# Performance work log

Hardware: AMD Instinct MI355X
Metric: run time of the kernel (lower is better)

Reference implementation:

```python
import jax, jax.numpy as jnp
import numpy as np

N = 2048
HID = 1024
Z = 256
DIM = 128 + 64 * 3 + 32 * 5  # 480
FAN = 128 * 128 + 64 * 64 + 32 * 32  # total fan-in over all CG paths


def _ln(x, g, b, eps=1e-6):
    mu = jnp.mean(x, axis=-1, keepdims=True)
    var = jnp.mean((x - mu) ** 2, axis=-1, keepdims=True)
    return (x - mu) * jax.lax.rsqrt(var + eps) * g + b


def _fctp(t, w0, w1, w2):
    # FullyConnectedTensorProduct(irreps, irreps, 'HIDx0e'):
    # only l1==l2 -> 0e paths survive; CG is delta_{m1,m2}/sqrt(2l+1).
    x0 = t[:, :128]                       # 128x0e
    x1 = t[:, 128:320].reshape(-1, 64, 3)  # 64x1o
    x2 = t[:, 320:480].reshape(-1, 32, 5)  # 32x2e
    e0 = jnp.einsum('bu,bv,uvh->bh', x0, x0, w0)
    e1 = jnp.einsum('bum,bvm,uvh->bh', x1, x1, w1) / np.sqrt(3.0)
    e2 = jnp.einsum('bum,bvm,uvh->bh', x2, x2, w2) / np.sqrt(5.0)
    return (e0 + e1 + e2) / np.sqrt(float(FAN))  # component normalization


def _head(t, w0, w1, w2, W1, b1, g1, be1, W2, b2, g2, be2):
    h = _fctp(t, w0, w1, w2)
    h = jax.nn.silu(_ln(h @ W1 + b1, g1, be1))
    h = jax.nn.silu(_ln(h @ W2 + b2, g2, be2))
    return h  # [N, Z]


def setup_inputs() -> dict:
    key = jax.random.key(0)
    ks = jax.random.split(key, 6)
    return {
        'tensor_in': jax.random.normal(ks[0], (N, DIM), jnp.float32),
        'w0': jax.random.normal(ks[1], (128, 128, HID), jnp.float32),
        'w1': jax.random.normal(ks[2], (64, 64, HID), jnp.float32),
        'w2': jax.random.normal(ks[3], (32, 32, HID), jnp.float32),
        'W1': jax.random.normal(ks[4], (HID, HID), jnp.float32) / np.sqrt(HID),
        'b1': jnp.zeros((HID,), jnp.float32),
        'g1': jnp.ones((HID,), jnp.float32),
        'be1': jnp.zeros((HID,), jnp.float32),
        'W2': jax.random.normal(ks[5], (HID, Z), jnp.float32) / np.sqrt(HID),
        'b2': jnp.zeros((Z,), jnp.float32),
        'g2': jnp.ones((Z,), jnp.float32),
        'be2': jnp.zeros((Z,), jnp.float32),
    }


def reference(tensor_in, w0, w1, w2, W1, b1, g1, be1, W2, b2, g2, be2):
    f = lambda t: _head(t, w0, w1, w2, W1, b1, g1, be1, W2, b2, g2, be2)
    x, pullback = jax.vjp(f, tensor_in)
    # torch: grad(x, tensor_in, grad_outputs=ones_like(x), create_graph=True)
    y = pullback(jnp.ones_like(x))[0]
    return x, y
```

## Files before the change

kernel.cpp:

```cpp
#include <hip/hip_runtime.h>
#include <math.h>

typedef unsigned short u16;
typedef __bf16 bf16x8 __attribute__((ext_vector_type(8)));
typedef float f32x4 __attribute__((ext_vector_type(4)));

#define NPACK  11264
#define NVALID 10864
#define BASE1  8256
#define BASE2  10336

__device__ __forceinline__ u16 f2bf(float f) {
    unsigned u = __builtin_bit_cast(unsigned, f);
    u += 0x7FFFu + ((u >> 16) & 1u);
    return (u16)(u >> 16);
}
__device__ __forceinline__ float bf2f(u16 h) {
    return __builtin_bit_cast(float, ((unsigned)h) << 16);
}

#define GLOAD_LDS16(g, l)                                                     \
    __builtin_amdgcn_global_load_lds(                                         \
        (const __attribute__((address_space(1))) void*)(g),                   \
        (__attribute__((address_space(3))) void*)(l), 16, 0, 0)

__device__ __forceinline__ int pk0(int a, int b) {
    int u = min(a, b), v = max(a, b);
    return u * 128 - (u * (u - 1)) / 2 + (v - u);
}
__device__ __forceinline__ int pk1(int a, int b) {
    int u = min(a, b), v = max(a, b);
    return BASE1 + u * 64 - (u * (u - 1)) / 2 + (v - u);
}
__device__ __forceinline__ int pk2(int a, int b) {
    int u = min(a, b), v = max(a, b);
    return BASE2 + u * 32 - (u * (u - 1)) / 2 + (v - u);
}

__global__ __launch_bounds__(256) void k_uvall(u16* __restrict__ tab) {
    int j = blockIdx.x * 256 + threadIdx.x;
    if (j < 16384) {
        int u = j >> 7, v = j & 127;
        if (v >= u) tab[pk0(u, v)] = (u16)((u << 7) | v);
    } else if (j < 20480) {
        int k = j - 16384, u = k >> 6, v = k & 63;
        if (v >= u) tab[pk1(u, v)] = (u16)((1 << 14) | (u << 7) | v);
    } else if (j < 21504) {
        int k = j - 20480, u = k >> 5, v = k & 31;
        if (v >= u) tab[pk2(u, v)] = (u16)((2 << 14) | (u << 7) | v);
    } else {
        int k = j - 21504;
        if (NVALID + k < NPACK) tab[NVALID + k] = 0xFFFFu;
    }
}

__global__ __launch_bounds__(256) void k_packw(const float* __restrict__ w0,
                                               const float* __restrict__ w1,
                                               const float* __restrict__ w2,
                                               const u16* __restrict__ tab,
                                               u16* __restrict__ Wsym,
                                               u16* __restrict__ Wt) {
    __shared__ u16 tile[32][258];
    __shared__ u16 te[32];
    int i0 = blockIdx.x * 32, h0 = blockIdx.y * 256, tid = threadIdx.x;
    if (tid < 32) te[tid] = tab[i0 + tid];
    __syncthreads();
    const float s1 = 0.57735026918962576f, s2 = 0.44721359549995794f;
    for (int il = 0; il < 32; il++) {
        unsigned e = te[il];
        float val = 0.f;
        if ((e >> 14) != 3) {
            int seg = e >> 14, u = (e >> 7) & 127, v = e & 127;
            const float* wb; int S; float sc;
            if (seg == 0)      { wb = w0; S = 128; sc = 1.f; }
            else if (seg == 1) { wb = w1; S = 64;  sc = s1; }
            else               { wb = w2; S = 32;  sc = s2; }
            val = sc * (wb[(size_t)(u * S + v) * 1024 + h0 + tid] +
                        wb[(size_t)(v * S + u) * 1024 + h0 + tid]);
        }
        u16 bv = f2bf(val);
        Wsym[(size_t)(i0 + il) * 1024 + h0 + tid] = bv;
        tile[il][tid] = bv;
    }
    __syncthreads();
    union { u16 a[32]; uint4 q[4]; } pk;
#pragma unroll
    for (int il = 0; il < 32; il++) pk.a[il] = tile[il][tid];
    uint4* dst = (uint4*)(Wt + (size_t)(h0 + tid) * NPACK + i0);
#pragma unroll
    for (int q = 0; q < 4; q++) dst[q] = pk.q[q];
}

__global__ __launch_bounds__(256) void k_convert(const float* __restrict__ in,
                                                 u16* __restrict__ out, int n4) {
    int i = blockIdx.x * 256 + threadIdx.x;
    if (i >= n4) return;
    float4 v = ((const float4*)in)[i];
    union { u16 a[4]; unsigned long long q; } o;
    o.a[0] = f2bf(v.x); o.a[1] = f2bf(v.y); o.a[2] = f2bf(v.z); o.a[3] = f2bf(v.w);
    ((unsigned long long*)out)[i] = o.q;
}

__global__ __launch_bounds__(256) void k_transpose(const float* __restrict__ in, int R, int C,
                                                   u16* __restrict__ out, int ldOut) {
    __shared__ float tile[32][33];
    int tr0 = blockIdx.y * 32;
    int tc0 = blockIdx.x * 32;
    int lr = threadIdx.x >> 5;
    int lc = threadIdx.x & 31;
#pragma unroll
    for (int i = 0; i < 4; i++) {
        int rr = lr + i * 8;
        tile[rr][lc] = in[(size_t)(tr0 + rr) * C + tc0 + lc];
    }
    __syncthreads();
#pragma unroll
    for (int i = 0; i < 4; i++) {
        int rr = lr + i * 8;
        out[(size_t)(tc0 + rr) * ldOut + tr0 + lc] = f2bf(tile[lc][rr]);
    }
}

__global__ __launch_bounds__(256) void k_features_pack(const float* __restrict__ t,
                                                       const u16* __restrict__ tab,
                                                       u16* __restrict__ P) {
    __shared__ u16 tab_s[NPACK];
    __shared__ float tr[480];
    int b = blockIdx.x, tid = threadIdx.x;
    for (int j = tid; j < NPACK / 8; j += 256)
        ((uint4*)tab_s)[j] = ((const uint4*)tab)[j];
    for (int j = tid; j < 480; j += 256) tr[j] = t[(size_t)b * 480 + j];
    __syncthreads();
    u16* row = P + (size_t)b * NPACK;
    for (int i = tid; i < NPACK; i += 256) {
        unsigned e = tab_s[i];
        float p = 0.f;
        if ((e >> 14) != 3) {
            int seg = e >> 14, u = (e >> 7) & 127, v = e & 127;
            if (seg == 0) p = tr[u] * tr[v];
            else if (seg == 1) {
                const float* x1 = tr + 128;
                p = x1[u*3]*x1[v*3] + x1[u*3+1]*x1[v*3+1] + x1[u*3+2]*x1[v*3+2];
            } else {
                const float* x2 = tr + 320;
#pragma unroll
                for (int m = 0; m < 5; m++) p += x2[u*5+m] * x2[v*5+m];
            }
            if (u == v) p *= 0.5f;
        }
        row[i] = f2bf(p);
    }
}

__global__ __launch_bounds__(256) void k_gemm2(const u16* __restrict__ A, int ldA,
                                               const u16* __restrict__ B, int ldB,
                                               int kLen, float scale,
                                               const float* __restrict__ bias,
                                               float* __restrict__ Cf,
                                               u16* __restrict__ Cb, int ldC,
                                               float* __restrict__ Cpart, int Mtot,
                                               int swz) {
    __shared__ u16 As[2][128 * 32];
    __shared__ u16 Bs[2][128 * 32];
    const int tid = threadIdx.x;
    const int wave = tid >> 6, lane = tid & 63;
    const int wm = wave >> 1, wn = wave & 1;
    int nT, mT, z;
    if (swz == 1) {
        int L = blockIdx.x;
        z = L & 7; int r = L >> 3;
        nT = r >> 4; mT = r & 15;
    } else if (swz == 2) {
        int L = blockIdx.x;
        int c = L & 7, r = L >> 3;
        nT = (r % 11) * 8 + c; mT = r / 11; z = 0;
    } else {
        nT = blockIdx.x; mT = blockIdx.y; z = blockIdx.z;
    }
    const int m0 = mT * 128, n0 = nT * 128;
    const size_t kOff = (size_t)z * kLen;

    const int chl = (((lane & 3) ^ ((lane >> 3) & 3))) * 8;
    const u16* aG = A + (size_t)(m0 + wave * 32 + (lane >> 2)) * ldA + kOff + chl;
    const u16* bG = B + (size_t)(n0 + wave * 32 + (lane >> 2)) * ldB + kOff + chl;
    const size_t aS = (size_t)16 * ldA;
    const size_t bS = (size_t)16 * ldB;
    u16* aL0 = &As[0][(wave * 32) * 32];
    u16* aL1 = &As[0][(wave * 32 + 16) * 32];
    u16* aH0 = &As[1][(wave * 32) * 32];
    u16* aH1 = &As[1][(wave * 32 + 16) * 32];
    u16* bL0 = &Bs[0][(wave * 32) * 32];
    u16* bL1 = &Bs[0][(wave * 32 + 16) * 32];
    u16* bH0 = &Bs[1][(wave * 32) * 32];
    u16* bH1 = &Bs[1][(wave * 32 + 16) * 32];

    f32x4 acc[4][4];
#pragma unroll
    for (int i = 0; i < 4; i++)
#pragma unroll
        for (int j = 0; j < 4; j++) acc[i][j] = (f32x4){0.f, 0.f, 0.f, 0.f};

    const int ml = lane & 15, kq8 = lane >> 4;
    const int kqs = (kq8 ^ ((ml >> 1) & 3)) * 8;
    const u16* aRd0 = &As[0][(wm * 64 + ml) * 32 + kqs];
    const u16* bRd0 = &Bs[0][(wn * 64 + ml) * 32 + kqs];
    const u16* aRd1 = &As[1][(wm * 64 + ml) * 32 + kqs];
    const u16* bRd1 = &Bs[1][(wn * 64 + ml) * 32 + kqs];

    for (int k = 0; k < kLen; k += 64) {
        GLOAD_LDS16(aG, aL0);
        GLOAD_LDS16(aG + aS, aL1);
        GLOAD_LDS16(aG + 32, aH0);
        GLOAD_LDS16(aG + aS + 32, aH1);
        GLOAD_LDS16(bG, bL0);
        GLOAD_LDS16(bG + bS, bL1);
        GLOAD_LDS16(bG + 32, bH0);
        GLOAD_LDS16(bG + bS + 32, bH1);
        aG += 64; bG += 64;
        __syncthreads();
        {
            bf16x8 af[4], bfv[4];
#pragma unroll
            for (int i = 0; i < 4; i++) af[i]  = *(const bf16x8*)(aRd0 + i * 16 * 32);
#pragma unroll
            for (int j = 0; j < 4; j++) bfv[j] = *(const bf16x8*)(bRd0 + j * 16 * 32);
#pragma unroll
            for (int i = 0; i < 4; i++)
#pragma unroll
                for (int j = 0; j < 4; j++)
                    acc[i][j] = __builtin_amdgcn_mfma_f32_16x16x32_bf16(af[i], bfv[j], acc[i][j], 0, 0, 0);
        }
        {
            bf16x8 af[4], bfv[4];
#pragma unroll
            for (int i = 0; i < 4; i++) af[i]  = *(const bf16x8*)(aRd1 + i * 16 * 32);
#pragma unroll
            for (int j = 0; j < 4; j++) bfv[j] = *(const bf16x8*)(bRd1 + j * 16 * 32);
#pragma unroll
            for (int i = 0; i < 4; i++)
#pragma unroll
                for (int j = 0; j < 4; j++)
                    acc[i][j] = __builtin_amdgcn_mfma_f32_16x16x32_bf16(af[i], bfv[j], acc[i][j], 0, 0, 0);
        }
        __syncthreads();
    }

    const int q = lane >> 4, nl = lane & 15;
    if (Cpart) {
        float* outP = Cpart + (size_t)z * Mtot * ldC;
#pragma unroll
        for (int i = 0; i < 4; i++)
#pragma unroll
            for (int j = 0; j < 4; j++)
#pragma unroll
                for (int reg = 0; reg < 4; reg++) {
                    int row = m0 + wm * 64 + i * 16 + q * 4 + reg;
                    int col = n0 + wn * 64 + j * 16 + nl;
                    outP[(size_t)row * ldC + col] = acc[i][j][reg];
                }
    } else {
#pragma unroll
        for (int i = 0; i < 4; i++)
#pragma unroll
            for (int j = 0; j < 4; j++)
#pragma unroll
                for (int reg = 0; reg < 4; reg++) {
                    int row = m0 + wm * 64 + i * 16 + q * 4 + reg;
                    int col = n0 + wn * 64 + j * 16 + nl;
                    float v = acc[i][j][reg] * scale + (bias ? bias[col] : 0.0f);
                    if (Cf) Cf[(size_t)row * ldC + col] = v;
                    else    Cb[(size_t)row * ldC + col] = f2bf(v);
                }
    }
}

#define VMCNT0 asm volatile("s_waitcnt vmcnt(0)" ::: "memory")
#define BARX() __builtin_amdgcn_s_barrier()

#define STG_A(p, kh, rh, kb) GLOAD_LDS16(aB + (size_t)(rh) * aH + (kb) + (kh) * 32, \
                                         &As[p][kh][((rh) * 128 + wave * 16) * 32])
#define STG_B(p, kh, rh, kb) GLOAD_LDS16(bB + (size_t)(rh) * bH + (kb) + (kh) * 32, \
                                         &Bs[p][kh][((rh) * 128 + wave * 16) * 32])
#define MMQ(fb, gb, bv) do { _Pragma("unroll") \
    for (int ff = 0; ff < 4; ff++) { _Pragma("unroll") \
        for (int gg = 0; gg < 2; gg++) { \
            acc[(fb)+ff][(gb)+gg] = __builtin_amdgcn_mfma_f32_16x16x32_bf16(a[2*ff],   bv[2*gg],   acc[(fb)+ff][(gb)+gg], 0, 0, 0); \
            acc[(fb)+ff][(gb)+gg] = __builtin_amdgcn_mfma_f32_16x16x32_bf16(a[2*ff+1], bv[2*gg+1], acc[(fb)+ff][(gb)+gg], 0, 0, 0); } } } while (0)

__global__ __launch_bounds__(512, 2) void k_gemm256(const u16* __restrict__ A, int ldA,
                                                    const u16* __restrict__ B, int ldB,
                                                    int kLen, float scale,
                                                    const float* __restrict__ bias,
                                                    u16* __restrict__ Cb, int ldC,
                                                    float* __restrict__ Cpart, int Mtot,
                                                    int swz) {
    __shared__ __align__(16) u16 As[2][2][256 * 32];
    __shared__ __align__(16) u16 Bs[2][2][256 * 32];
    const int tid = threadIdx.x;
    const int lane = tid & 63, wave = tid >> 6;
    const int wm = wave >> 2, wn = wave & 3;
    int mT, nT, z;
    if (swz == 1) {
        z = blockIdx.x & 7; int r = blockIdx.x >> 3; nT = r & 3; mT = r >> 2;
    } else {
        int x = blockIdx.x & 7, j = blockIdx.x >> 3;
        int nti = j >> 3; mT = j & 7;
        if (nti < 5)      nT = nti * 8 + x;
        else if (x < 4)   nT = 40 + x;
        else            { nT = 40 + (x - 4); mT = (j & 7) + 4; }
        z = 0;
    }
    const int m0 = mT * 256, n0 = nT * 256;
    const size_t kOff = (size_t)z * kLen;
    const int nTi = kLen >> 6;

    const int chl = ((tid & 3) ^ ((tid >> 3) & 3)) * 8;
    const u16* aB = A + (size_t)(m0 + (tid >> 2)) * ldA + kOff + chl;
    const u16* bB = B + (size_t)(n0 + (tid >> 2)) * ldB + kOff + chl;
    const size_t aH = (size_t)128 * ldA;
    const size_t bH = (size_t)128 * ldB;

    const int ml = lane & 15, kq8 = lane >> 4;
    const int kqs = (kq8 ^ ((ml >> 1) & 3)) * 8;
    const int aro = (wm * 128 + ml) * 32 + kqs;
    const int bro = (wn * 64 + ml) * 32 + kqs;

    f32x4 acc[8][4];
#pragma unroll
    for (int f = 0; f < 8; f++)
#pragma unroll
        for (int g = 0; g < 4; g++) acc[f][g] = (f32x4){0.f, 0.f, 0.f, 0.f};
    bf16x8 a[8], b[4], b2[4];

    STG_A(0, 0, 0, 0); STG_A(0, 0, 1, 0); STG_A(0, 1, 0, 0); STG_A(0, 1, 1, 0);
    STG_B(0, 0, 0, 0); STG_B(0, 0, 1, 0); STG_B(0, 1, 0, 0); STG_B(0, 1, 1, 0);
    VMCNT0;
    BARX();

    for (int t = 0; t < nTi; t++) {
        const int p = t & 1, p1 = p ^ 1;
        const int kb1 = (t + 1) << 6;
        const bool s1 = (t + 1) < nTi;
#pragma unroll
        for (int f = 0; f < 4; f++) {
            a[2*f]   = *(const bf16x8*)&As[p][0][aro + f * 512];
            a[2*f+1] = *(const bf16x8*)&As[p][1][aro + f * 512];
        }
#pragma unroll
        for (int g = 0; g < 2; g++) {
            b[2*g]   = *(const bf16x8*)&Bs[p][0][bro + g * 512];
            b[2*g+1] = *(const bf16x8*)&Bs[p][1][bro + g * 512];
        }
        if (s1) { STG_A(p1, 0, 0, kb1); STG_A(p1, 0, 1, kb1); }
        BARX();
        __builtin_amdgcn_s_setprio(1);
        MMQ(0, 0, b);
        __builtin_amdgcn_s_setprio(0);
        BARX();
#pragma unroll
        for (int g = 0; g < 2; g++) {
            b2[2*g]   = *(const bf16x8*)&Bs[p][0][bro + (g + 2) * 512];
            b2[2*g+1] = *(const bf16x8*)&Bs[p][1][bro + (g + 2) * 512];
        }
        if (s1) { STG_A(p1, 1, 0, kb1); STG_A(p1, 1, 1, kb1); }
        BARX();
        __builtin_amdgcn_s_setprio(1);
        MMQ(0, 2, b2);
        __builtin_amdgcn_s_setprio(0);
        BARX();
#pragma unroll
        for (int f = 0; f < 4; f++) {
            a[2*f]   = *(const bf16x8*)&As[p][0][aro + (f + 4) * 512];
            a[2*f+1] = *(const bf16x8*)&As[p][1][aro + (f + 4) * 512];
        }
        if (s1) { STG_B(p1, 0, 0, kb1); STG_B(p1, 0, 1, kb1); }
        BARX();
        __builtin_amdgcn_s_setprio(1);
        MMQ(4, 0, b);
        __builtin_amdgcn_s_setprio(0);
        BARX();
        if (s1) { STG_B(p1, 1, 0, kb1); STG_B(p1, 1, 1, kb1); }
        __builtin_amdgcn_s_setprio(1);
        MMQ(4, 2, b2);
        __builtin_amdgcn_s_setprio(0);
        if (s1) VMCNT0;
        BARX();
    }

    const int q = lane >> 4, nl = lane & 15;
    if (Cpart) {
        float* outP = Cpart + (size_t)z * Mtot * ldC;
#pragma unroll
        for (int f = 0; f < 8; f++)
#pragma unroll
            for (int g = 0; g < 4; g++)
#pragma unroll
                for (int reg = 0; reg < 4; reg++) {
                    int row = m0 + wm * 128 + f * 16 + q * 4 + reg;
                    int col = n0 + wn * 64 + g * 16 + nl;
                    outP[(size_t)row * ldC + col] = acc[f][g][reg];
                }
    } else {
#pragma unroll
        for (int f = 0; f < 8; f++)
#pragma unroll
            for (int g = 0; g < 4; g++)
#pragma unroll
                for (int reg = 0; reg < 4; reg++) {
                    int row = m0 + wm * 128 + f * 16 + q * 4 + reg;
                    int col = n0 + wn * 64 + g * 16 + nl;
                    float v = acc[f][g][reg] * scale + (bias ? bias[col] : 0.0f);
                    Cb[(size_t)row * ldC + col] = f2bf(v);
                }
    }
}

__global__ __launch_bounds__(256) void k_reduce(const float* __restrict__ part, size_t stride,
                                                int SK, int total, int N, float scale,
                                                const float* __restrict__ bias,
                                                float* __restrict__ outF, u16* __restrict__ outB) {
    int i = blockIdx.x * 256 + threadIdx.x;
    if (i >= total) return;
    float s = 0.f;
    for (int z = 0; z < SK; z++) s += part[(size_t)z * stride + i];
    float v = s * scale + (bias ? bias[i % N] : 0.0f);
    if (outF) outF[i] = v;
    else      outB[i] = f2bf(v);
}

__device__ __forceinline__ float blockReduce(float v, float* red) {
#pragma unroll
    for (int off = 32; off > 0; off >>= 1) v += __shfl_down(v, off);
    __syncthreads();
    if ((threadIdx.x & 63) == 0) red[threadIdx.x >> 6] = v;
    __syncthreads();
    return red[0] + red[1] + red[2] + red[3];
}

__global__ __launch_bounds__(256) void k_ln_fwd(const float* __restrict__ X, int D,
    const float* __restrict__ g, const float* __restrict__ be,
    float* __restrict__ mu_out, float* __restrict__ r_out,
    u16* __restrict__ a_bf, float* __restrict__ a_f32) {
    __shared__ float red[4];
    int b = blockIdx.x, tid = threadIdx.x;
    const float* x = X + (size_t)b * D;
    int nd = D >> 8;
    float s = 0.f, s2 = 0.f;
    for (int r = 0; r < nd; r++) { float v = x[tid + (r << 8)]; s += v; s2 += v * v; }
    s = blockReduce(s, red);
    s2 = blockReduce(s2, red);
    float mu = s / D;
    float var = s2 / D - mu * mu;
    float rst = rsqrtf(var + 1e-6f);
    if (tid == 0) { mu_out[b] = mu; r_out[b] = rst; }
    for (int r = 0; r < nd; r++) {
        int i = tid + (r << 8);
        float xh = (x[i] - mu) * rst;
        float ln = xh * g[i] + be[i];
        float a = ln / (1.0f + expf(-ln));
        if (a_bf)  a_bf[(size_t)b * D + i] = f2bf(a);
        if (a_f32) a_f32[(size_t)b * D + i] = a;
    }
}

__global__ __launch_bounds__(256) void k_ln_bwd(const float* __restrict__ dup,
    const float* __restrict__ X, const float* __restrict__ mu_in, const float* __restrict__ r_in,
    const float* __restrict__ g, const float* __restrict__ be,
    u16* __restrict__ out_bf, int D) {
    __shared__ float red[4];
    int b = blockIdx.x, tid = threadIdx.x;
    const float* x = X + (size_t)b * D;
    float mu = mu_in[b], rst = r_in[b];
    int nd = D >> 8;
    float w_[4], xh_[4];
    float sw = 0.f, swx = 0.f;
    for (int r = 0; r < nd; r++) {
        int i = tid + (r << 8);
        float xh = (x[i] - mu) * rst;
        float ln = xh * g[i] + be[i];
        float sg = 1.0f / (1.0f + expf(-ln));
        float dsilu = sg * (1.0f + ln * (1.0f - sg));
        float d = dup ? dup[(size_t)b * D + i] : 1.0f;
        float w = g[i] * dsilu * d;
        w_[r] = w; xh_[r] = xh;
        sw += w; swx += w * xh;
    }
    sw = blockReduce(sw, red);
    swx = blockReduce(swx, red);
    float invD = 1.0f / D;
    for (int r = 0; r < nd; r++) {
        int i = tid + (r << 8);
        float dx = rst * (w_[r] - sw * invD - xh_[r] * swx * invD);
        out_bf[(size_t)b * D + i] = f2bf(dx);
    }
}

__global__ __launch_bounds__(256) void k_contract_p(const u16* __restrict__ Gp,
                                                    const float* __restrict__ t,
                                                    float* __restrict__ y) {
    __shared__ u16 gp_s[NPACK];
    __shared__ float xs[480];
    int b = blockIdx.x, tid = threadIdx.x;
    const uint4* gsrc = (const uint4*)(Gp + (size_t)b * NPACK);
    for (int j = tid; j < NPACK / 8; j += 256) ((uint4*)gp_s)[j] = gsrc[j];
    for (int j = tid; j < 480; j += 256) xs[j] = t[(size_t)b * 480 + j];
    __syncthreads();
    int wave = tid >> 6, lane = tid & 63;
    float* yr = y + (size_t)b * 480;
    for (int r = 0; r < 32; r++) {
        int u = wave * 32 + r;
        int v0 = lane, v1 = lane + 64;
        float s = bf2f(gp_s[pk0(u, v0)]) * xs[v0] + bf2f(gp_s[pk0(u, v1)]) * xs[v1];
#pragma unroll
        for (int off = 32; off > 0; off >>= 1) s += __shfl_down(s, off);
        if (lane == 0) yr[u] = s;
    }
    for (int r = 0; r < 16; r++) {
        int u = wave * 16 + r;
        float gv = bf2f(gp_s[pk1(u, lane)]);
        float a0 = gv * xs[128 + lane * 3 + 0];
        float a1 = gv * xs[128 + lane * 3 + 1];
        float a2 = gv * xs[128 + lane * 3 + 2];
#pragma unroll
        for (int off = 32; off > 0; off >>= 1) {
            a0 += __shfl_down(a0, off);
            a1 += __shfl_down(a1, off);
            a2 += __shfl_down(a2, off);
        }
        if (lane == 0) {
            yr[128 + u * 3 + 0] = a0;
            yr[128 + u * 3 + 1] = a1;
            yr[128 + u * 3 + 2] = a2;
        }
    }
    for (int r = 0; r < 8; r++) {
        int u = wave * 8 + r;
        bool act = lane < 32;
        float gv = act ? bf2f(gp_s[pk2(u, act ? lane : 0)]) : 0.f;
        float a[5];
#pragma unroll
        for (int m = 0; m < 5; m++)
            a[m] = act ? gv * xs[320 + lane * 5 + m] : 0.f;
#pragma unroll
        for (int off = 32; off > 0; off >>= 1)
#pragma unroll
            for (int m = 0; m < 5; m++) a[m] += __shfl_down(a[m], off);
        if (lane == 0)
#pragma unroll
            for (int m = 0; m < 5; m++) yr[320 + u * 5 + m] = a[m];
    }
}

extern "C" void kernel_launch(void* const* d_in, const int* in_sizes, int n_in,
                              void* d_out, int out_size, void* d_ws, size_t ws_size,
                              hipStream_t stream) {
    const float* t   = (const float*)d_in[0];
    const float* w0  = (const float*)d_in[1];
    const float* w1  = (const float*)d_in[2];
    const float* w2  = (const float*)d_in[3];
    const float* W1  = (const float*)d_in[4];
    const float* b1  = (const float*)d_in[5];
    const float* g1  = (const float*)d_in[6];
    const float* be1 = (const float*)d_in[7];
    const float* W2  = (const float*)d_in[8];
    const float* b2  = (const float*)d_in[9];
    const float* g2  = (const float*)d_in[10];
    const float* be2 = (const float*)d_in[11];

    float* xout = (float*)d_out;
    float* yout = xout + (size_t)2048 * 256;

    char* ws = (char*)d_ws;
    size_t off = 0;
    auto alloc = [&](size_t bytes) -> void* {
        void* p = ws + off;
        off += (bytes + 255) & ~(size_t)255;
        return p;
    };
    u16*   PG    = (u16*)alloc((size_t)2048 * NPACK * 2);
    u16*   Wsym  = (u16*)alloc((size_t)NPACK * 1024 * 2);
    u16*   Wt    = (u16*)alloc((size_t)1024 * NPACK * 2);
    u16*   uvtab = (u16*)alloc((size_t)NPACK * 2);
    u16*   W1b   = (u16*)alloc((size_t)1024 * 1024 * 2);
    u16*   W1tb  = (u16*)alloc((size_t)1024 * 1024 * 2);
    u16*   W2b   = (u16*)alloc((size_t)1024 * 256 * 2);
    u16*   W2tb  = (u16*)alloc((size_t)256 * 1024 * 2);
    u16*   h_bf  = (u16*)alloc((size_t)2048 * 1024 * 2);
    float* h1pre = (float*)alloc((size_t)2048 * 1024 * 4);
    float* mu1   = (float*)alloc(2048 * 4);
    float* r1    = (float*)alloc(2048 * 4);
    u16*   a1_bf = (u16*)alloc((size_t)2048 * 1024 * 2);
    float* h2pre = (float*)alloc((size_t)2048 * 256 * 4);
    float* mu2   = (float*)alloc(2048 * 4);
    float* r2    = (float*)alloc(2048 * 4);
    u16*   dh2b  = (u16*)alloc((size_t)2048 * 256 * 2);
    float* d_a1  = (float*)alloc((size_t)2048 * 1024 * 4);
    u16*   dh1b  = (u16*)alloc((size_t)2048 * 1024 * 2);
    u16*   de_bf = (u16*)alloc((size_t)2048 * 1024 * 2);
    float* Cpart = (float*)(ws + off);
    size_t cpartBytes = (ws_size > off) ? (ws_size - off) : 0;
    (void)in_sizes; (void)n_in; (void)out_size;

    const float sF = 1.0f / sqrtf(21504.0f);

    auto gemm = [&](const u16* A, int ldA, const u16* B, int ldB, int M, int N, int K,
                    int SKwant, float scale, const float* bias,
                    float* Cf, u16* Cb, int ldC) {
        int SK = SKwant;
        size_t slice = (size_t)M * ldC * 4;
        if (SK > 1 && cpartBytes < 2 * slice) SK = 1;
        if (SK > 1 && (size_t)SK * slice > cpartBytes) SK = (int)(cpartBytes / slice);
        while (SK > 1 && !((K % SK) == 0 && ((K / SK) % 64) == 0)) SK--;
        dim3 grid(N / 128, M / 128, SK);
        if (SK > 1) {
            k_gemm2<<<grid, 256, 0, stream>>>(A, ldA, B, ldB, K / SK, 0.f, nullptr,
                                              nullptr, nullptr, ldC, Cpart, M, 0);
            int total = M * ldC;
            k_reduce<<<(total + 255) / 256, 256, 0, stream>>>(Cpart, (size_t)M * ldC, SK,
                                                              total, N, scale, bias, Cf, Cb);
        } else {
            k_gemm2<<<grid, 256, 0, stream>>>(A, ldA, B, ldB, K, scale, bias,
                                              Cf, Cb, ldC, nullptr, M, 0);
        }
    };

    k_uvall<<<(21504 + NPACK - NVALID + 255) / 256, 256, 0, stream>>>(uvtab);
    k_packw<<<dim3(NPACK / 32, 4), 256, 0, stream>>>(w0, w1, w2, uvtab, Wsym, Wt);

    k_transpose<<<dim3(32, 32), 256, 0, stream>>>(W1, 1024, 1024, W1tb, 1024);
    k_transpose<<<dim3(8, 32), 256, 0, stream>>>(W2, 1024, 256, W2tb, 1024);
    k_convert<<<1024 * 1024 / 1024, 256, 0, stream>>>(W1, W1b, 1024 * 1024 / 4);
    k_convert<<<1024 * 256 / 1024, 256, 0, stream>>>(W2, W2b, 1024 * 256 / 4);

    k_features_pack<<<2048, 256, 0, stream>>>(t, uvtab, PG);

    k_gemm256<<<dim3(256), 512, 0, stream>>>(PG, NPACK, Wt, NPACK, NPACK / 8, 0.f, nullptr,
                                             nullptr, 1024, Cpart, 2048, 1);
    {
        int total = 2048 * 1024;
        k_reduce<<<(total + 255) / 256, 256, 0, stream>>>(Cpart, (size_t)2048 * 1024, 8,
                                                          total, 1024, sF, nullptr,
                                                          nullptr, h_bf);
    }

    gemm(h_bf, 1024, W1tb, 1024, 2048, 1024, 1024, 4, 1.0f, b1, h1pre, nullptr, 1024);
    k_ln_fwd<<<2048, 256, 0, stream>>>(h1pre, 1024, g1, be1, mu1, r1, a1_bf, nullptr);
    gemm(a1_bf, 1024, W2tb, 1024, 2048, 256, 1024, 8, 1.0f, b2, h2pre, nullptr, 256);
    k_ln_fwd<<<2048, 256, 0, stream>>>(h2pre, 256, g2, be2, mu2, r2, nullptr, xout);

    k_ln_bwd<<<2048, 256, 0, stream>>>(nullptr, h2pre, mu2, r2, g2, be2, dh2b, 256);
    gemm(dh2b, 256, W2b, 256, 2048, 1024, 256, 4, 1.0f, nullptr, d_a1, nullptr, 1024);
    k_ln_bwd<<<2048, 256, 0, stream>>>(d_a1, h1pre, mu1, r1, g1, be1, dh1b, 1024);
    gemm(dh1b, 1024, W1b, 1024, 2048, 1024, 1024, 4, sF, nullptr, nullptr, de_bf, 1024);

    u16* Gp = PG;
    k_gemm256<<<dim3(352), 512, 0, stream>>>(de_bf, 1024, Wsym, 1024, 1024, 1.0f, nullptr,
                                             Gp, NPACK, nullptr, 2048, 2);

    k_contract_p<<<2048, 256, 0, stream>>>(Gp, t, yout);
}
```

Baseline: 515.7 us.

## Merge weight prep kernels into one launch and store split-K partials as bf16

Five small preprocessing launches (index table, W1/W2 transposes and conversions) become a single kernel that picks its role from the block index, cutting launch overhead. Separately, the split-K GEMM partial sums are now written and read as bf16 instead of fp32, halving partial-buffer traffic. This also changes the workspace sizing so more split slices may fit. The cost is extra rounding of each partial before reduction, which lowers accuracy.

```diff
diff --git a/kernel.cpp b/kernel.cpp
--- a/kernel.cpp
+++ b/kernel.cpp
@@ -37,20 +37,65 @@
     return BASE2 + u * 32 - (u * (u - 1)) / 2 + (v - u);
 }
 
-__global__ __launch_bounds__(256) void k_uvall(u16* __restrict__ tab) {
-    int j = blockIdx.x * 256 + threadIdx.x;
-    if (j < 16384) {
-        int u = j >> 7, v = j & 127;
-        if (v >= u) tab[pk0(u, v)] = (u16)((u << 7) | v);
-    } else if (j < 20480) {
-        int k = j - 16384, u = k >> 6, v = k & 63;
-        if (v >= u) tab[pk1(u, v)] = (u16)((1 << 14) | (u << 7) | v);
-    } else if (j < 21504) {
-        int k = j - 20480, u = k >> 5, v = k & 31;
-        if (v >= u) tab[pk2(u, v)] = (u16)((2 << 14) | (u << 7) | v);
+__device__ __forceinline__ void prep_transpose(const float* __restrict__ in, int C,
+                                               u16* __restrict__ out, int ldOut,
+                                               int bx, int by, int tid) {
+    __shared__ float tile[32][33];
+    int tr0 = by * 32, tc0 = bx * 32;
+    int lr = tid >> 5, lc = tid & 31;
+#pragma unroll
+    for (int i = 0; i < 4; i++) {
+        int rr = lr + i * 8;
+        tile[rr][lc] = in[(size_t)(tr0 + rr) * C + tc0 + lc];
+    }
+    __syncthreads();
+#pragma unroll
+    for (int i = 0; i < 4; i++) {
+        int rr = lr + i * 8;
+        out[(size_t)(tc0 + rr) * ldOut + tr0 + lc] = f2bf(tile[lc][rr]);
+    }
+}
+__device__ __forceinline__ void prep_convert(const float* __restrict__ in,
+                                             u16* __restrict__ out, int i, int n4) {
+    if (i >= n4) return;
+    float4 v = ((const float4*)in)[i];
+    union { u16 a[4]; unsigned long long q; } o;
+    o.a[0] = f2bf(v.x); o.a[1] = f2bf(v.y); o.a[2] = f2bf(v.z); o.a[3] = f2bf(v.w);
+    ((unsigned long long*)out)[i] = o.q;
+}
+
+__global__ __launch_bounds__(256) void k_prep(u16* __restrict__ tab,
+                                              const float* __restrict__ W1,
+                                              const float* __restrict__ W2,
+                                              u16* __restrict__ W1b,
+                                              u16* __restrict__ W1tb,
+                                              u16* __restrict__ W2b,
+                                              u16* __restrict__ W2tb) {
+    int bid = blockIdx.x, tid = threadIdx.x;
+    if (bid < 86) {
+        int j = bid * 256 + tid;
+        if (j < 16384) {
+            int u = j >> 7, v = j & 127;
+            if (v >= u) tab[pk0(u, v)] = (u16)((u << 7) | v);
+        } else if (j < 20480) {
+            int k = j - 16384, u = k >> 6, v = k & 63;
+            if (v >= u) tab[pk1(u, v)] = (u16)((1 << 14) | (u << 7) | v);
+        } else if (j < 21504) {
+            int k = j - 20480, u = k >> 5, v = k & 31;
+            if (v >= u) tab[pk2(u, v)] = (u16)((2 << 14) | (u << 7) | v);
+        } else if (j < 21504 + (NPACK - NVALID)) {
+            tab[NVALID + (j - 21504)] = 0xFFFFu;
+        }
+    } else if (bid < 1110) {
+        int k = bid - 86;
+        prep_transpose(W1, 1024, W1tb, 1024, k & 31, k >> 5, tid);
+    } else if (bid < 1366) {
+        int k = bid - 1110;
+        prep_transpose(W2, 256, W2tb, 1024, k & 7, k >> 3, tid);
+    } else if (bid < 2390) {
+        prep_convert(W1, W1b, (bid - 1366) * 256 + tid, 1024 * 1024 / 4);
     } else {
-        int k = j - 21504;
-        if (NVALID + k < NPACK) tab[NVALID + k] = 0xFFFFu;
+        prep_convert(W2, W2b, (bid - 2390) * 256 + tid, 1024 * 256 / 4);
     }
 }
 
@@ -91,36 +136,6 @@
     for (int q = 0; q < 4; q++) dst[q] = pk.q[q];
 }
 
-__global__ __launch_bounds__(256) void k_convert(const float* __restrict__ in,
-                                                 u16* __restrict__ out, int n4) {
-    int i = blockIdx.x * 256 + threadIdx.x;
-    if (i >= n4) return;
-    float4 v = ((const float4*)in)[i];
-    union { u16 a[4]; unsigned long long q; } o;
-    o.a[0] = f2bf(v.x); o.a[1] = f2bf(v.y); o.a[2] = f2bf(v.z); o.a[3] = f2bf(v.w);
-    ((unsigned long long*)out)[i] = o.q;
-}
-
-__global__ __launch_bounds__(256) void k_transpose(const float* __restrict__ in, int R, int C,
-                                                   u16* __restrict__ out, int ldOut) {
-    __shared__ float tile[32][33];
-    int tr0 = blockIdx.y * 32;
-    int tc0 = blockIdx.x * 32;
-    int lr = threadIdx.x >> 5;
-    int lc = threadIdx.x & 31;
-#pragma unroll
-    for (int i = 0; i < 4; i++) {
-        int rr = lr + i * 8;
-        tile[rr][lc] = in[(size_t)(tr0 + rr) * C + tc0 + lc];
-    }
-    __syncthreads();
-#pragma unroll
-    for (int i = 0; i < 4; i++) {
-        int rr = lr + i * 8;
-        out[(size_t)(tc0 + rr) * ldOut + tr0 + lc] = f2bf(tile[lc][rr]);
-    }
-}
-
 __global__ __launch_bounds__(256) void k_features_pack(const float* __restrict__ t,
                                                        const u16* __restrict__ tab,
                                                        u16* __restrict__ P) {
@@ -158,7 +173,7 @@
                                                const float* __restrict__ bias,
                                                float* __restrict__ Cf,
                                                u16* __restrict__ Cb, int ldC,
-                                               float* __restrict__ Cpart, int Mtot,
+                                               u16* __restrict__ Cpart, int Mtot,
                                                int swz) {
     __shared__ u16 As[2][128 * 32];
     __shared__ u16 Bs[2][128 * 32];
@@ -247,7 +262,7 @@
 
     const int q = lane >> 4, nl = lane & 15;
     if (Cpart) {
-        float* outP = Cpart + (size_t)z * Mtot * ldC;
+        u16* outP = Cpart + (size_t)z * Mtot * ldC;
 #pragma unroll
         for (int i = 0; i < 4; i++)
 #pragma unroll
@@ -256,7 +271,7 @@
                 for (int reg = 0; reg < 4; reg++) {
                     int row = m0 + wm * 64 + i * 16 + q * 4 + reg;
                     int col = n0 + wn * 64 + j * 16 + nl;
-                    outP[(size_t)row * ldC + col] = acc[i][j][reg];
+                    outP[(size_t)row * ldC + col] = f2bf(acc[i][j][reg]);
                 }
     } else {
 #pragma unroll
@@ -292,7 +307,7 @@
                                                     int kLen, float scale,
                                                     const float* __restrict__ bias,
                                                     u16* __restrict__ Cb, int ldC,
-                                                    float* __restrict__ Cpart, int Mtot,
+                                                    u16* __restrict__ Cpart, int Mtot,
                                                     int swz) {
     __shared__ __align__(16) u16 As[2][2][256 * 32];
     __shared__ __align__(16) u16 Bs[2][2][256 * 32];
@@ -389,7 +404,7 @@
 
     const int q = lane >> 4, nl = lane & 15;
     if (Cpart) {
-        float* outP = Cpart + (size_t)z * Mtot * ldC;
+        u16* outP = Cpart + (size_t)z * Mtot * ldC;
 #pragma unroll
         for (int f = 0; f < 8; f++)
 #pragma unroll
@@ -398,7 +413,7 @@
                 for (int reg = 0; reg < 4; reg++) {
                     int row = m0 + wm * 128 + f * 16 + q * 4 + reg;
                     int col = n0 + wn * 64 + g * 16 + nl;
-                    outP[(size_t)row * ldC + col] = acc[f][g][reg];
+                    outP[(size_t)row * ldC + col] = f2bf(acc[f][g][reg]);
                 }
     } else {
 #pragma unroll
@@ -415,14 +430,14 @@
     }
 }
 
-__global__ __launch_bounds__(256) void k_reduce(const float* __restrict__ part, size_t stride,
+__global__ __launch_bounds__(256) void k_reduce(const u16* __restrict__ part, size_t stride,
                                                 int SK, int total, int N, float scale,
                                                 const float* __restrict__ bias,
                                                 float* __restrict__ outF, u16* __restrict__ outB) {
     int i = blockIdx.x * 256 + threadIdx.x;
     if (i >= total) return;
     float s = 0.f;
-    for (int z = 0; z < SK; z++) s += part[(size_t)z * stride + i];
+    for (int z = 0; z < SK; z++) s += bf2f(part[(size_t)z * stride + i]);
     float v = s * scale + (bias ? bias[i % N] : 0.0f);
     if (outF) outF[i] = v;
     else      outB[i] = f2bf(v);
@@ -597,7 +612,7 @@
     float* d_a1  = (float*)alloc((size_t)2048 * 1024 * 4);
     u16*   dh1b  = (u16*)alloc((size_t)2048 * 1024 * 2);
     u16*   de_bf = (u16*)alloc((size_t)2048 * 1024 * 2);
-    float* Cpart = (float*)(ws + off);
+    u16*   Cpart = (u16*)(ws + off);
     size_t cpartBytes = (ws_size > off) ? (ws_size - off) : 0;
     (void)in_sizes; (void)n_in; (void)out_size;
 
@@ -607,7 +622,7 @@
                     int SKwant, float scale, const float* bias,
                     float* Cf, u16* Cb, int ldC) {
         int SK = SKwant;
-        size_t slice = (size_t)M * ldC * 4;
+        size_t slice = (size_t)M * ldC * 2;
         if (SK > 1 && cpartBytes < 2 * slice) SK = 1;
         if (SK > 1 && (size_t)SK * slice > cpartBytes) SK = (int)(cpartBytes / slice);
         while (SK > 1 && !((K % SK) == 0 && ((K / SK) % 64) == 0)) SK--;
@@ -624,13 +639,8 @@
         }
     };
 
-    k_uvall<<<(21504 + NPACK - NVALID + 255) / 256, 256, 0, stream>>>(uvtab);
+    k_prep<<<2646, 256, 0, stream>>>(uvtab, W1, W2, W1b, W1tb, W2b, W2tb);
     k_packw<<<dim3(NPACK / 32, 4), 256, 0, stream>>>(w0, w1, w2, uvtab, Wsym, Wt);
-
-    k_transpose<<<dim3(32, 32), 256, 0, stream>>>(W1, 1024, 1024, W1tb, 1024);
-    k_transpose<<<dim3(8, 32), 256, 0, stream>>>(W2, 1024, 256, W2tb, 1024);
-    k_convert<<<1024 * 1024 / 1024, 256, 0, stream>>>(W1, W1b, 1024 * 1024 / 4);
-    k_convert<<<1024 * 256 / 1024, 256, 0, stream>>>(W2, W2b, 1024 * 256 / 4);
 
     k_features_pack<<<2048, 256, 0, stream>>>(t, uvtab, PG);
 
```

Measured after the change: 501.1 us. 2.8% less time.
